# Kernel tuning notes

Measured on AMD Instinct MI355X. Metric: run time of the kernel, lower is better.

The kernel has to match this reference:

```python
import jax, jax.numpy as jnp
import numpy as np

HEADS = 8
DIM_HEAD = 128
ATTN_MATRIX_SCALE = 1.5  # tau applied to mean-centered logits
SCALE = DIM_HEAD ** -0.5


def setup_inputs() -> dict:
    key = jax.random.key(0)
    ks = jax.random.split(key, 7)
    b, n, m = 2, 2048, 2048
    qd, cd, inner = 1024, 768, HEADS * DIM_HEAD
    x = jax.random.normal(ks[0], (b, n, qd), dtype=jnp.float32)
    context = jax.random.normal(ks[1], (b, m, cd), dtype=jnp.float32)
    Wq = jax.random.normal(ks[2], (qd, inner), dtype=jnp.float32) * (qd ** -0.5)
    Wk = jax.random.normal(ks[3], (cd, inner), dtype=jnp.float32) * (cd ** -0.5)
    Wv = jax.random.normal(ks[4], (cd, inner), dtype=jnp.float32) * (cd ** -0.5)
    Wout = jax.random.normal(ks[5], (inner, qd), dtype=jnp.float32) * (inner ** -0.5)
    bout = jnp.zeros((qd,), dtype=jnp.float32)
    return {"x": x, "context": context, "Wq": Wq, "Wk": Wk, "Wv": Wv,
            "Wout": Wout, "bout": bout}


def _split_heads(t):
    # (b, n, h*d) -> (h, b*n, d); matches rearrange '(b h) n d -> h (b n) d'
    b, n, _ = t.shape
    t = t.reshape(b, n, HEADS, DIM_HEAD)
    return t.transpose(2, 0, 1, 3).reshape(HEADS, b * n, DIM_HEAD)


def reference(x, context, Wq, Wk, Wv, Wout, bout):
    b, n, _ = x.shape
    qh = _split_heads(jnp.einsum('bnq,qi->bni', x, Wq))        # (h, b*n, d)
    kh = _split_heads(jnp.einsum('bmc,ci->bmi', context, Wk))  # (h, b*m, d)
    vh = _split_heads(jnp.einsum('bmc,ci->bmi', context, Wv))  # (h, b*m, d)

    # custom mean-centered / tau-scaled similarity (_compute_sim_with_tau)
    sim = jnp.einsum('hid,hjd->hij', qh, kh) * SCALE
    mean = jnp.mean(sim, axis=-1, keepdims=True)
    sim = (sim - mean) * ATTN_MATRIX_SCALE + mean

    attn = jax.nn.softmax(sim, axis=-1)
    out = jnp.einsum('hij,hjd->hid', attn, vh)                 # (h, b*n, d)

    # (h, b*n, d) -> (b, n, h*d)
    out = out.reshape(HEADS, b, n, DIM_HEAD).transpose(1, 2, 0, 3)
    out = out.reshape(b, n, HEADS * DIM_HEAD)
    return jnp.einsum('bni,iq->bnq', out, Wout) + bout
```

## Files before the change

### kernel.cpp

```cpp
#include <hip/hip_runtime.h>
#include <cstdint>
#include <cstddef>

typedef unsigned short u16t;
typedef __bf16 bf16x8_t __attribute__((ext_vector_type(8)));
typedef float f32x4_t __attribute__((ext_vector_type(4)));
typedef float f32x16_t __attribute__((ext_vector_type(16)));

#define MFMA_BF16 __builtin_amdgcn_mfma_f32_16x16x32_bf16
#define MFMA32    __builtin_amdgcn_mfma_f32_32x32x16_bf16

__device__ __forceinline__ u16t f2bf(float f) {
    uint32_t u = __builtin_bit_cast(uint32_t, f);
    u += 0x7fffu + ((u >> 16) & 1u);
    return (u16t)(u >> 16);
}

__device__ __forceinline__ uint32_t pk2bf(float a, float b) {
    return (uint32_t)f2bf(a) | ((uint32_t)f2bf(b) << 16);
}

__device__ __forceinline__ float bflo(uint32_t u) {
    return __builtin_bit_cast(float, u << 16);
}
__device__ __forceinline__ float bfhi(uint32_t u) {
    return __builtin_bit_cast(float, u & 0xffff0000u);
}

__device__ __forceinline__ bf16x8_t ld_frag(const u16t* p) {
    return __builtin_bit_cast(bf16x8_t, *(const uint4*)p);
}

__device__ __forceinline__ uint32_t cvtpk(float lo, float hi) {
    uint32_t r;
    asm("v_cvt_pk_bf16_f32 %0, %1, %2" : "=v"(r) : "v"(lo), "v"(hi));
    return r;
}
__device__ __forceinline__ void swap32(uint32_t& a, uint32_t& b) {
    asm("v_permlane32_swap_b32 %0, %1" : "+v"(a), "+v"(b));
}

__device__ __forceinline__ void gl_lds16(const u16t* g, u16t* l) {
    __builtin_amdgcn_global_load_lds(
        (const __attribute__((address_space(1))) void*)g,
        (__attribute__((address_space(3))) void*)l, 16, 0, 0);
}

__global__ void cast2_bf16_kernel(const float* __restrict__ s0, u16t* __restrict__ d0, int n0,
                                  const float* __restrict__ s1, u16t* __restrict__ d1, int n1) {
    int i = blockIdx.x * blockDim.x + threadIdx.x;
    const float* s; u16t* d;
    if (i < n0) { s = s0; d = d0; }
    else { i -= n0; if (i >= n1) return; s = s1; d = d1; }
    float4 v = ((const float4*)s)[i];
    uint2 o;
    o.x = pk2bf(v.x, v.y);
    o.y = pk2bf(v.z, v.w);
    ((uint2*)d)[i] = o;
}

__global__ void transpose4_kernel(const float* __restrict__ Wq, const float* __restrict__ Wk,
                                  const float* __restrict__ Wv, const float* __restrict__ Wo,
                                  u16t* __restrict__ Wqt, u16t* __restrict__ Wkt,
                                  u16t* __restrict__ Wvt, u16t* __restrict__ Wot) {
    const int z = blockIdx.z;
    const float* W = z == 0 ? Wq : (z == 1 ? Wk : (z == 2 ? Wv : Wo));
    u16t* Wt      = z == 0 ? Wqt : (z == 1 ? Wkt : (z == 2 ? Wvt : Wot));
    const int K   = (z == 1 || z == 2) ? 768 : 1024;
    const int N = 1024;
    int n0 = blockIdx.x * 32, k0 = blockIdx.y * 32;
    if (k0 >= K) return;
    __shared__ float tile[32][33];
    int tx = threadIdx.x, ty = threadIdx.y;
    for (int i = ty; i < 32; i += 8)
        tile[i][tx] = W[(size_t)(k0 + i) * N + n0 + tx];
    __syncthreads();
    for (int i = ty; i < 32; i += 8)
        Wt[(size_t)(n0 + i) * K + k0 + tx] = f2bf(tile[tx][i]);
}

__device__ __forceinline__ void gemm_core(
    const u16t* __restrict__ A, const u16t* __restrict__ Bt,
    int K, void* __restrict__ outp, const float* __restrict__ bias,
    int mode, float oscale, int bm, int bn)
{
    __shared__ __align__(16) u16t As[2][128 * 64];
    __shared__ __align__(16) u16t Bs[2][64 * 64];
    const int tid = threadIdx.x;
    const int wave = tid >> 6, lane = tid & 63;
    const int wm = wave & 1, wn = wave >> 1;
    const int quad = lane >> 4, l16 = lane & 15;

    const int l8r = lane >> 3, l8c = lane & 7;
    const int cgx = (l8c ^ l8r) * 8;

    f32x4_t acc[4][2];
#pragma unroll
    for (int i = 0; i < 4; ++i)
#pragma unroll
        for (int j = 0; j < 2; ++j) acc[i][j] = (f32x4_t){0.f, 0.f, 0.f, 0.f};

    const int nk = K >> 6;

#pragma unroll
    for (int it = 0; it < 4; ++it) {
        int rb = wave * 32 + it * 8;
        gl_lds16(&A[(size_t)(bm + rb + l8r) * K + cgx], &As[0][rb * 64]);
    }
#pragma unroll
    for (int it = 0; it < 2; ++it) {
        int rb = wave * 16 + it * 8;
        gl_lds16(&Bt[(size_t)(bn + rb + l8r) * K + cgx], &Bs[0][rb * 64]);
    }

    for (int ki = 0; ki < nk; ++ki) {
        const int buf = ki & 1;
        __syncthreads();

        if (ki + 1 < nk) {
            const int kc = (ki + 1) << 6;
#pragma unroll
            for (int it = 0; it < 4; ++it) {
                int rb = wave * 32 + it * 8;
                gl_lds16(&A[(size_t)(bm + rb + l8r) * K + kc + cgx], &As[buf ^ 1][rb * 64]);
            }
#pragma unroll
            for (int it = 0; it < 2; ++it) {
                int rb = wave * 16 + it * 8;
                gl_lds16(&Bt[(size_t)(bn + rb + l8r) * K + kc + cgx], &Bs[buf ^ 1][rb * 64]);
            }
        }

#pragma unroll
        for (int ks = 0; ks < 2; ++ks) {
            bf16x8_t af[4], bfv[2];
#pragma unroll
            for (int i = 0; i < 4; ++i) {
                int r = wm * 64 + i * 16 + l16;
                af[i] = ld_frag(&As[buf][r * 64 + (((ks * 4 + quad) ^ (r & 7)) * 8)]);
            }
#pragma unroll
            for (int j = 0; j < 2; ++j) {
                int r = wn * 32 + j * 16 + l16;
                bfv[j] = ld_frag(&Bs[buf][r * 64 + (((ks * 4 + quad) ^ (r & 7)) * 8)]);
            }
#pragma unroll
            for (int i = 0; i < 4; ++i)
#pragma unroll
                for (int j = 0; j < 2; ++j)
                    acc[i][j] = MFMA_BF16(af[i], bfv[j], acc[i][j], 0, 0, 0);
        }
    }

    if (mode == 3) {
        float* out = (float*)outp;
#pragma unroll
        for (int j = 0; j < 2; ++j) {
            int c = bn + wn * 32 + j * 16 + l16;
            float b = bias[c];
#pragma unroll
            for (int i = 0; i < 4; ++i) {
                int rb = bm + wm * 64 + i * 16 + quad * 4;
#pragma unroll
                for (int r = 0; r < 4; ++r)
                    out[(size_t)(rb + r) * 1024 + c] = acc[i][j][r] + b;
            }
        }
    } else if (mode == 2) {
        u16t* out = (u16t*)outp;
#pragma unroll
        for (int i = 0; i < 4; ++i)
#pragma unroll
            for (int j = 0; j < 2; ++j) {
                int rb = bm + wm * 64 + i * 16 + quad * 4;
                int c = bn + wn * 32 + j * 16 + l16;
                int h = c >> 7, d = c & 127;
                uint2 pk;
                pk.x = pk2bf(acc[i][j][0], acc[i][j][1]);
                pk.y = pk2bf(acc[i][j][2], acc[i][j][3]);
                *(uint2*)&out[((size_t)h * 128 + d) * 4096 + rb] = pk;
            }
    } else {
        u16t* out = (u16t*)outp;
#pragma unroll
        for (int i = 0; i < 4; ++i)
#pragma unroll
            for (int j = 0; j < 2; ++j) {
                int rb = bm + wm * 64 + i * 16 + quad * 4;
                int c = bn + wn * 32 + j * 16 + l16;
                int h = c >> 7, d = c & 127;
#pragma unroll
                for (int r = 0; r < 4; ++r)
                    out[((size_t)h * 4096 + rb + r) * 128 + d] = f2bf(acc[i][j][r] * oscale);
            }
    }
}

__global__ __launch_bounds__(256) void gemm_bf16_kernel(
    const u16t* __restrict__ A, const u16t* __restrict__ Bt,
    int K, void* __restrict__ outp, const float* __restrict__ bias,
    int mode, float oscale)
{
    gemm_core(A, Bt, K, outp, bias, mode, oscale, blockIdx.y * 128, blockIdx.x * 64);
}

__global__ __launch_bounds__(256) void qkv_kernel(
    const u16t* __restrict__ x_bf, const u16t* __restrict__ ctx_bf,
    const u16t* __restrict__ Wqt, const u16t* __restrict__ Wkt,
    const u16t* __restrict__ Wvt,
    u16t* __restrict__ Qh, u16t* __restrict__ Kh, u16t* __restrict__ Vt,
    float qscale)
{
    const int z = blockIdx.z;
    const u16t* A  = (z == 0) ? x_bf : ctx_bf;
    const u16t* Bt = (z == 0) ? Wqt : ((z == 1) ? Wkt : Wvt);
    void* outp     = (z == 0) ? (void*)Qh : ((z == 1) ? (void*)Kh : (void*)Vt);
    const int K    = (z == 0) ? 1024 : 768;
    const int mode = (z == 2) ? 2 : 0;
    const float sc = (z == 0) ? qscale : 1.0f;
    gemm_core(A, Bt, K, outp, nullptr, mode, sc, blockIdx.y * 128, blockIdx.x * 64);
}

__global__ __launch_bounds__(256, 2) void flash_kernel(
    const u16t* __restrict__ Qh, const u16t* __restrict__ Kh,
    const u16t* __restrict__ Vtg, u16t* __restrict__ Op0,
    u16t* __restrict__ Op1, float* __restrict__ lp)
{
    extern __shared__ __align__(16) u16t smem[];
    const int h = blockIdx.y;
    const int q0 = blockIdx.x * 128;
    const int z = blockIdx.z;
    const int tid = threadIdx.x;
    const int wave = tid >> 6, lane = tid & 63;
    const int l31 = lane & 31, hh = lane >> 5;
    const int NT = 32;

    const u16t* Kg = Kh + (size_t)h * 4096 * 128 + (size_t)z * 2048 * 128;
    const u16t* Vg = Vtg + (size_t)h * 128 * 4096 + z * 2048;

    {
        const u16t* Qg = Qh + ((size_t)h * 4096 + q0) * 128;
#pragma unroll
        for (int it = 0; it < 8; ++it) {
            int slot = it * 256 + tid;
            int r = slot >> 4, c = slot & 15;
            uint4 v = *(const uint4*)&Qg[(size_t)r * 128 + c * 8];
            *(uint4*)&smem[r * 128 + ((c ^ (r & 15)) * 8)] = v;
        }
    }
    __syncthreads();
    bf16x8_t qf[8];
    {
        int r = wave * 32 + l31;
#pragma unroll
        for (int s = 0; s < 8; ++s)
            qf[s] = ld_frag(&smem[r * 128 + (((s * 2 + hh) ^ (r & 15)) * 8)]);
    }
    __syncthreads();

    const bool kRole = wave < 2;
    const int wh = wave & 1;
    const int rK = lane >> 4, cK = lane & 15;
    const int rV = lane >> 3, cV = lane & 7;

    if (kRole) {
#pragma unroll
        for (int it = 0; it < 8; ++it) {
            int is = wh * 8 + it;
            int rowL = is * 4 + rK;
            gl_lds16(Kg + (size_t)rowL * 128 + ((cK ^ (rowL & 15)) * 8),
                     smem + is * 512);
        }
    }

    f32x16_t Ow[4];
#pragma unroll
    for (int dg = 0; dg < 4; ++dg)
#pragma unroll
        for (int r = 0; r < 16; ++r) Ow[dg][r] = 0.f;

    float lsum = 0.f;
    const int swzk = l31 & 15;
    bf16x8_t pf[4];

    for (int t = 0; t <= NT; ++t) {
        __syncthreads();

        if (kRole) {
            if (t + 1 < NT) {
                const int j0 = (t + 1) * 64;
                u16t* kd = smem + ((t + 1) & 1) * 8192;
#pragma unroll
                for (int it = 0; it < 8; ++it) {
                    int is = wh * 8 + it;
                    int rowL = is * 4 + rK;
                    gl_lds16(Kg + (size_t)(j0 + rowL) * 128 + ((cK ^ (rowL & 15)) * 8),
                             kd + is * 512);
                }
            }
        } else {
            if (t < NT) {
                const int j0 = t * 64;
                u16t* vd = smem + 16384 + (t & 1) * 8192;
#pragma unroll
                for (int it = 0; it < 8; ++it) {
                    int is = wh * 8 + it;
                    int rowL = is * 8 + rV;
                    gl_lds16(Vg + (size_t)rowL * 4096 + j0 + ((cV ^ ((rowL ^ (rowL >> 3)) & 7)) * 8),
                             vd + is * 512);
                }
            }
        }

        __builtin_amdgcn_s_setprio(1);
        f32x16_t St0, St1;
#pragma unroll
        for (int r = 0; r < 16; ++r) { St0[r] = 0.f; St1[r] = 0.f; }
        if (t < NT) {
            const u16t* kb = smem + (t & 1) * 8192;
#pragma unroll
            for (int s = 0; s < 8; ++s) {
                int ch = ((s * 2 + hh) ^ swzk) * 8;
                bf16x8_t k0 = ld_frag(&kb[l31 * 128 + ch]);
                bf16x8_t k1 = ld_frag(&kb[(32 + l31) * 128 + ch]);
                St0 = MFMA32(k0, qf[s], St0, 0, 0, 0);
                St1 = MFMA32(k1, qf[s], St1, 0, 0, 0);
            }
        }
        if (t >= 1) {
            const u16t* vb = smem + 16384 + ((t - 1) & 1) * 8192;
#pragma unroll
            for (int dg = 0; dg < 4; ++dg) {
                int rv = dg * 32 + l31;
                int gsw = (rv ^ (rv >> 3)) & 7;
#pragma unroll
                for (int sl = 0; sl < 4; ++sl) {
                    bf16x8_t vf = ld_frag(&vb[rv * 64 + (((sl * 2 + hh) ^ gsw) * 8)]);
                    Ow[dg] = MFMA32(vf, pf[sl], Ow[dg], 0, 0, 0);
                }
            }
        }
        __builtin_amdgcn_s_setprio(0);

        if (t < NT) {
#pragma unroll
            for (int half = 0; half < 2; ++half) {
                float p[16];
#pragma unroll
                for (int r = 0; r < 16; ++r)
                    p[r] = __builtin_amdgcn_exp2f(half ? St1[r] : St0[r]);
                lsum += ((((p[0] + p[1]) + (p[2] + p[3])) + ((p[4] + p[5]) + (p[6] + p[7])))
                      + (((p[8] + p[9]) + (p[10] + p[11])) + ((p[12] + p[13]) + (p[14] + p[15]))));
                uint32_t w0 = cvtpk(p[0], p[1]),   w2 = cvtpk(p[4], p[5]);
                uint32_t w1 = cvtpk(p[2], p[3]),   w3 = cvtpk(p[6], p[7]);
                swap32(w0, w2); swap32(w1, w3);
                uint32_t y0 = cvtpk(p[8], p[9]),   y2 = cvtpk(p[12], p[13]);
                uint32_t y1 = cvtpk(p[10], p[11]), y3 = cvtpk(p[14], p[15]);
                swap32(y0, y2); swap32(y1, y3);
                uint4 pw0; pw0.x = w0; pw0.y = w1; pw0.z = w2; pw0.w = w3;
                uint4 pw1; pw1.x = y0; pw1.y = y1; pw1.z = y2; pw1.w = y3;
                pf[half * 2 + 0] = __builtin_bit_cast(bf16x8_t, pw0);
                pf[half * 2 + 1] = __builtin_bit_cast(bf16x8_t, pw1);
            }
        }
    }

    lsum += __shfl_xor(lsum, 32, 64);
    u16t* Op = z ? Op1 : Op0;
    size_t i = (size_t)(q0 + wave * 32 + l31);
    if (hh == 0) lp[z * 32768 + i * 8 + h] = lsum;
#pragma unroll
    for (int dg = 0; dg < 4; ++dg)
#pragma unroll
        for (int g = 0; g < 4; ++g) {
            uint2 pk;
            pk.x = pk2bf(Ow[dg][g * 4 + 0], Ow[dg][g * 4 + 1]);
            pk.y = pk2bf(Ow[dg][g * 4 + 2], Ow[dg][g * 4 + 3]);
            *(uint2*)&Op[i * 1024 + h * 128 + dg * 32 + g * 8 + hh * 4] = pk;
        }
}

__global__ __launch_bounds__(256) void combine_kernel(
    const u16t* __restrict__ O0, const u16t* __restrict__ O1,
    const float* __restrict__ lp, u16t* __restrict__ out)
{
    int t = blockIdx.x * blockDim.x + threadIdx.x;
    int e = t << 3;
    int i = e >> 10, h = (e >> 7) & 7;
    float inv = 1.f / (lp[i * 8 + h] + lp[32768 + i * 8 + h]);
    uint4 a = ((const uint4*)O0)[t];
    uint4 b = ((const uint4*)O1)[t];
    uint4 r;
    r.x = pk2bf((bflo(a.x) + bflo(b.x)) * inv, (bfhi(a.x) + bfhi(b.x)) * inv);
    r.y = pk2bf((bflo(a.y) + bflo(b.y)) * inv, (bfhi(a.y) + bfhi(b.y)) * inv);
    r.z = pk2bf((bflo(a.z) + bflo(b.z)) * inv, (bfhi(a.z) + bfhi(b.z)) * inv);
    r.w = pk2bf((bflo(a.w) + bflo(b.w)) * inv, (bfhi(a.w) + bfhi(b.w)) * inv);
    ((uint4*)out)[t] = r;
}

extern "C" void kernel_launch(void* const* d_in, const int* in_sizes, int n_in,
                              void* d_out, int out_size, void* d_ws, size_t ws_size,
                              hipStream_t stream)
{
    (void)in_sizes; (void)n_in; (void)out_size; (void)ws_size;
    const float* x    = (const float*)d_in[0];
    const float* ctx  = (const float*)d_in[1];
    const float* Wq   = (const float*)d_in[2];
    const float* Wk   = (const float*)d_in[3];
    const float* Wv   = (const float*)d_in[4];
    const float* Wout = (const float*)d_in[5];
    const float* bout = (const float*)d_in[6];
    float* out = (float*)d_out;

    u16t* ws = (u16t*)d_ws;
    u16t* x_bf   = ws;
    u16t* ctx_bf = x_bf + 4194304;
    u16t* Wqt    = ctx_bf + 3145728;
    u16t* Wkt    = Wqt + 1048576;
    u16t* Wvt    = Wkt + 786432;
    u16t* Woutt  = Wvt + 786432;
    u16t* Qh     = Woutt + 1048576;
    u16t* Kh     = Qh + 4194304;
    u16t* Vt     = Kh + 4194304;
    u16t* Oh   = x_bf;
    u16t* Ohp1 = ws + 4194304;
    float* lp  = (float*)(ws + 8388608);

    constexpr float QSCALE = 1.5f * 0.08838834764831845f * 1.4426950408889634f;

    (void)hipFuncSetAttribute((const void*)flash_kernel,
                              hipFuncAttributeMaxDynamicSharedMemorySize, 65536);

    cast2_bf16_kernel<<<7168, 256, 0, stream>>>(x, x_bf, 1048576, ctx, ctx_bf, 786432);
    transpose4_kernel<<<dim3(32, 32, 4), dim3(32, 8), 0, stream>>>(
        Wq, Wk, Wv, Wout, Wqt, Wkt, Wvt, Woutt);

    qkv_kernel<<<dim3(16, 32, 3), 256, 0, stream>>>(
        x_bf, ctx_bf, Wqt, Wkt, Wvt, Qh, Kh, Vt, QSCALE);

    flash_kernel<<<dim3(32, 8, 2), 256, 65536, stream>>>(Qh, Kh, Vt, Oh, Ohp1, lp);
    combine_kernel<<<2048, 256, 0, stream>>>(Oh, Ohp1, lp, Oh);

    gemm_bf16_kernel<<<dim3(16, 32), 256, 0, stream>>>(Oh, Woutt, 1024, out, bout, 3, 1.0f);
}
```

Before: 234.6 us.

## Replace QKV projection with dedicated 128x128-tile kernel using 32x32 MFMA and async LDS loads

The shared 128x64 GEMM core used for the Q/K/V projections is replaced with a dedicated kernel that uses 128x128 tiles (one head per block column). It uses 32x32x16 bf16 MFMA, double-buffered direct global-to-LDS loads with a swizzled layout, and split producer roles (two waves load A, two load B). The larger tile raises arithmetic intensity and halves the block count. In exchange it needs 64 KB of dynamic LDS and a two-blocks-per-CU bound, which could limit occupancy. The now-unused mode 0/2 epilogues are removed from the generic GEMM core.

```diff
diff --git a/kernel.cpp b/kernel.cpp
--- a/kernel.cpp
+++ b/kernel.cpp
@@ -166,33 +166,6 @@
                     out[(size_t)(rb + r) * 1024 + c] = acc[i][j][r] + b;
             }
         }
-    } else if (mode == 2) {
-        u16t* out = (u16t*)outp;
-#pragma unroll
-        for (int i = 0; i < 4; ++i)
-#pragma unroll
-            for (int j = 0; j < 2; ++j) {
-                int rb = bm + wm * 64 + i * 16 + quad * 4;
-                int c = bn + wn * 32 + j * 16 + l16;
-                int h = c >> 7, d = c & 127;
-                uint2 pk;
-                pk.x = pk2bf(acc[i][j][0], acc[i][j][1]);
-                pk.y = pk2bf(acc[i][j][2], acc[i][j][3]);
-                *(uint2*)&out[((size_t)h * 128 + d) * 4096 + rb] = pk;
-            }
-    } else {
-        u16t* out = (u16t*)outp;
-#pragma unroll
-        for (int i = 0; i < 4; ++i)
-#pragma unroll
-            for (int j = 0; j < 2; ++j) {
-                int rb = bm + wm * 64 + i * 16 + quad * 4;
-                int c = bn + wn * 32 + j * 16 + l16;
-                int h = c >> 7, d = c & 127;
-#pragma unroll
-                for (int r = 0; r < 4; ++r)
-                    out[((size_t)h * 4096 + rb + r) * 128 + d] = f2bf(acc[i][j][r] * oscale);
-            }
     }
 }
 
@@ -204,21 +177,121 @@
     gemm_core(A, Bt, K, outp, bias, mode, oscale, blockIdx.y * 128, blockIdx.x * 64);
 }
 
-__global__ __launch_bounds__(256) void qkv_kernel(
+__global__ __launch_bounds__(256, 2) void qkv128_kernel(
     const u16t* __restrict__ x_bf, const u16t* __restrict__ ctx_bf,
     const u16t* __restrict__ Wqt, const u16t* __restrict__ Wkt,
     const u16t* __restrict__ Wvt,
     u16t* __restrict__ Qh, u16t* __restrict__ Kh, u16t* __restrict__ Vt,
     float qscale)
 {
+    extern __shared__ __align__(16) u16t sm[];
     const int z = blockIdx.z;
     const u16t* A  = (z == 0) ? x_bf : ctx_bf;
     const u16t* Bt = (z == 0) ? Wqt : ((z == 1) ? Wkt : Wvt);
-    void* outp     = (z == 0) ? (void*)Qh : ((z == 1) ? (void*)Kh : (void*)Vt);
     const int K    = (z == 0) ? 1024 : 768;
-    const int mode = (z == 2) ? 2 : 0;
     const float sc = (z == 0) ? qscale : 1.0f;
-    gemm_core(A, Bt, K, outp, nullptr, mode, sc, blockIdx.y * 128, blockIdx.x * 64);
+    const int m0 = blockIdx.y * 128;
+    const int h  = blockIdx.x;
+
+    const int tid = threadIdx.x;
+    const int wave = tid >> 6, lane = tid & 63;
+    const int l31 = lane & 31, hh = lane >> 5;
+    const int wm = wave & 1, wn = wave >> 1;
+    const bool aRole = wave < 2;
+    const int wh = wave & 1;
+    const int rS = lane >> 3, cS = lane & 7;
+
+    const int nk = K >> 6;
+    const u16t* G  = aRole ? A : Bt;
+    const int base = aRole ? m0 : h * 128;
+    u16t* dstb     = sm + (aRole ? 0 : 16384);
+
+#pragma unroll
+    for (int it = 0; it < 8; ++it) {
+        int is = wh * 8 + it;
+        int rowL = is * 8 + rS;
+        gl_lds16(&G[(size_t)(base + rowL) * K + ((cS ^ ((rowL ^ (rowL >> 3)) & 7)) * 8)],
+                 dstb + is * 512);
+    }
+
+    f32x16_t acc[2][2];
+#pragma unroll
+    for (int i = 0; i < 2; ++i)
+#pragma unroll
+        for (int j = 0; j < 2; ++j)
+#pragma unroll
+            for (int r = 0; r < 16; ++r) acc[i][j][r] = 0.f;
+
+    for (int ki = 0; ki < nk; ++ki) {
+        const int buf = ki & 1;
+        __syncthreads();
+
+        if (ki + 1 < nk) {
+            const int kc = (ki + 1) << 6;
+            u16t* dst = dstb + (buf ^ 1) * 8192;
+#pragma unroll
+            for (int it = 0; it < 8; ++it) {
+                int is = wh * 8 + it;
+                int rowL = is * 8 + rS;
+                gl_lds16(&G[(size_t)(base + rowL) * K + kc + ((cS ^ ((rowL ^ (rowL >> 3)) & 7)) * 8)],
+                         dst + is * 512);
+            }
+        }
+
+        const u16t* As = sm + buf * 8192;
+        const u16t* Bs = sm + 16384 + buf * 8192;
+        __builtin_amdgcn_s_setprio(1);
+#pragma unroll
+        for (int s = 0; s < 4; ++s) {
+            bf16x8_t af[2], bfr[2];
+#pragma unroll
+            for (int i = 0; i < 2; ++i) {
+                int r = wm * 64 + i * 32 + l31;
+                af[i] = ld_frag(&As[r * 64 + (((s * 2 + hh) ^ ((r ^ (r >> 3)) & 7)) * 8)]);
+            }
+#pragma unroll
+            for (int j = 0; j < 2; ++j) {
+                int r = wn * 64 + j * 32 + l31;
+                bfr[j] = ld_frag(&Bs[r * 64 + (((s * 2 + hh) ^ ((r ^ (r >> 3)) & 7)) * 8)]);
+            }
+#pragma unroll
+            for (int i = 0; i < 2; ++i)
+#pragma unroll
+                for (int j = 0; j < 2; ++j)
+                    acc[i][j] = MFMA32(af[i], bfr[j], acc[i][j], 0, 0, 0);
+        }
+        __builtin_amdgcn_s_setprio(0);
+    }
+
+    if (z != 2) {
+        u16t* out = (z == 0) ? Qh : Kh;
+#pragma unroll
+        for (int i = 0; i < 2; ++i)
+#pragma unroll
+            for (int j = 0; j < 2; ++j) {
+                int d = wn * 64 + j * 32 + l31;
+#pragma unroll
+                for (int g = 0; g < 16; ++g) {
+                    int m = m0 + wm * 64 + i * 32 + (g & 3) + 8 * (g >> 2) + 4 * hh;
+                    out[((size_t)h * 4096 + m) * 128 + d] = f2bf(acc[i][j][g] * sc);
+                }
+            }
+    } else {
+#pragma unroll
+        for (int i = 0; i < 2; ++i)
+#pragma unroll
+            for (int j = 0; j < 2; ++j) {
+                int d = wn * 64 + j * 32 + l31;
+                size_t vb = ((size_t)h * 128 + d) * 4096 + m0 + wm * 64 + i * 32;
+#pragma unroll
+                for (int gq = 0; gq < 4; ++gq) {
+                    uint2 pk;
+                    pk.x = pk2bf(acc[i][j][gq * 4 + 0], acc[i][j][gq * 4 + 1]);
+                    pk.y = pk2bf(acc[i][j][gq * 4 + 2], acc[i][j][gq * 4 + 3]);
+                    *(uint2*)&Vt[vb + gq * 8 + 4 * hh] = pk;
+                }
+            }
+    }
 }
 
 __global__ __launch_bounds__(256, 2) void flash_kernel(
@@ -430,12 +503,14 @@
 
     (void)hipFuncSetAttribute((const void*)flash_kernel,
                               hipFuncAttributeMaxDynamicSharedMemorySize, 65536);
+    (void)hipFuncSetAttribute((const void*)qkv128_kernel,
+                              hipFuncAttributeMaxDynamicSharedMemorySize, 65536);
 
     cast2_bf16_kernel<<<7168, 256, 0, stream>>>(x, x_bf, 1048576, ctx, ctx_bf, 786432);
     transpose4_kernel<<<dim3(32, 32, 4), dim3(32, 8), 0, stream>>>(
         Wq, Wk, Wv, Wout, Wqt, Wkt, Wvt, Woutt);
 
-    qkv_kernel<<<dim3(16, 32, 3), 256, 0, stream>>>(
+    qkv128_kernel<<<dim3(8, 32, 3), 256, 65536, stream>>>(
         x_bf, ctx_bf, Wqt, Wkt, Wvt, Qh, Kh, Vt, QSCALE);
 
     flash_kernel<<<dim3(32, 8, 2), 256, 65536, stream>>>(Qh, Kh, Vt, Oh, Ohp1, lp);
```

New measurement: 229.6 us. 2.1% less time.
